# Kernel tuning notes

Measured on AMD Instinct MI355X. Metric: run time of the kernel, lower is better.

The kernel has to match this reference:

```python
import jax, jax.numpy as jnp
import numpy as np


def setup_inputs() -> dict:
    key = jax.random.key(0)
    ks = jax.random.split(key, 7)
    B, C, H, W = 8, 512, 32, 32
    N = 4
    Cn = C // N
    return {
        "first": jax.random.normal(ks[0], (B, C, H, W), dtype=jnp.float32),
        "second": jax.random.normal(ks[1], (B, C, H, W), dtype=jnp.float32),
        "w1": jax.random.normal(ks[2], (Cn, Cn), dtype=jnp.float32) * 0.05,
        "w2": jax.random.normal(ks[3], (Cn, Cn), dtype=jnp.float32) * 0.05,
        "w3": jax.random.normal(ks[4], (Cn, Cn), dtype=jnp.float32) * 0.05,
        "w4": jax.random.normal(ks[5], (Cn, Cn), dtype=jnp.float32) * 0.05,
        "w5": jax.random.normal(ks[6], (C, N), dtype=jnp.float32) * 0.05,
        "head_count": N,
    }


def reference(first, second, w1, w2, w3, w4, w5, head_count):
    B, C, H, W = first.shape
    N = head_count
    Cn = C // N
    L = H * W
    f = first.reshape(B * N, Cn, L)   # [BN, Cn, L]
    s = second.reshape(B * N, Cn, L)
    # 1x1 convs (no bias) == channel matmuls
    key_t = jnp.einsum('oc,bcl->blo', w1, f)    # [BN, L, Cn]
    query = jnp.einsum('oc,bcl->bol', w2, s)    # [BN, Cn, L]
    scores = jnp.einsum('blc,bcm->blm', key_t, query)  # [BN, L, L]
    attn = jax.nn.softmax(scores, axis=2)
    v1_t = jnp.einsum('oc,bcl->blo', w3, f)     # [BN, L, Cn]
    v2 = jnp.einsum('oc,bcl->bol', w4, s)       # [BN, Cn, L]
    value = jnp.einsum('blc,bcm->blm', v1_t, v2)  # [BN, L, L]
    res = jnp.sum(attn * value, axis=2)         # [BN, L]
    res = res.reshape(B, N, H, W)
    out = jax.nn.relu(jnp.einsum('on,bnhw->bohw', w5, res))  # [B, C, H, W]
    return out
```

## Files before the change

kernel.cpp:

```cpp
#include <hip/hip_runtime.h>
#include <hip/hip_bf16.h>
#include <stdint.h>

constexpr int BN = 32;
constexpr int Cn = 128;
constexpr int L  = 1024;
constexpr int CC = 512;
constexpr int BB = 8;

typedef __bf16 bf16x8 __attribute__((ext_vector_type(8)));
typedef float  f32x4  __attribute__((ext_vector_type(4)));
typedef unsigned short u16x8 __attribute__((ext_vector_type(8)));

__device__ inline unsigned short f2bf(float f) {
    unsigned int x = __float_as_uint(f);
    x += 0x7fffu + ((x >> 16) & 1u);
    return (unsigned short)(x >> 16);
}

__device__ inline void gl_lds16(const void* g, void* l) {
    typedef __attribute__((address_space(1))) const unsigned int GU;
    typedef __attribute__((address_space(3))) unsigned int LU;
    __builtin_amdgcn_global_load_lds((GU*)g, (LU*)l, 16, 0, 0);
}

__global__ __launch_bounds__(256)
void wsplit_kernel(const float* __restrict__ w1, const float* __restrict__ w2,
                   const float* __restrict__ w3, const float* __restrict__ w4,
                   unsigned short* __restrict__ whi, unsigned short* __restrict__ wlo)
{
    int idx = (blockIdx.x * 256 + threadIdx.x) * 4;
    int mat = idx >> 14;
    int off = idx & 16383;
    const float* w = (mat == 0) ? w1 : (mat == 1) ? w2 : (mat == 2) ? w3 : w4;
    float4 v = *(const float4*)&w[off];
    ushort4 hi, lo;
    hi.x = f2bf(v.x); lo.x = f2bf(v.x - __uint_as_float((unsigned)hi.x << 16));
    hi.y = f2bf(v.y); lo.y = f2bf(v.y - __uint_as_float((unsigned)hi.y << 16));
    hi.z = f2bf(v.z); lo.z = f2bf(v.z - __uint_as_float((unsigned)hi.z << 16));
    hi.w = f2bf(v.w); lo.w = f2bf(v.w - __uint_as_float((unsigned)hi.w << 16));
    *(ushort4*)&whi[idx] = hi;
    *(ushort4*)&wlo[idx] = lo;
}

__global__ __launch_bounds__(512, 2)
void proj_kernel(const float* __restrict__ first, const float* __restrict__ second,
                 const unsigned short* __restrict__ whi,
                 const unsigned short* __restrict__ wlo,
                 unsigned short* __restrict__ outP)
{
    __shared__ unsigned short xs[2][2][64 * 128];

    const int p   = blockIdx.x;
    const int lq  = p & 3;
    const int src = (p >> 2) & 1;
    const int bn  = p >> 3;

    const float* x = (src == 0 ? first : second) + (size_t)bn * Cn * L + lq * 256;

    const int tid  = threadIdx.x;
    const int lane = tid & 63;
    const int wv   = tid >> 6;
    const int mat  = wv & 1;
    const int oh   = (wv >> 1) & 1;
    const int lh   = wv >> 2;
    const int r16  = lane & 15;
    const int g    = lane >> 4;

    const int mi = mat * 2 + src;
    const unsigned short* WHm = whi + mi * 16384;
    const unsigned short* WLm = wlo + mi * 16384;
    unsigned short* Pout = outP + (size_t)(mi * BN + bn) * (L * Cn);

    bf16x8 ah[4][4], al[4][4];
    #pragma unroll
    for (int og = 0; og < 4; ++og)
        #pragma unroll
        for (int kk = 0; kk < 4; ++kk) {
            int o = oh * 64 + og * 16 + r16;
            int c = kk * 32 + g * 8;
            ah[og][kk] = *(const bf16x8*)&WHm[o * 128 + c];
            al[og][kk] = *(const bf16x8*)&WLm[o * 128 + c];
        }

    const int sl   = tid & 63;
    const int cblk = tid >> 6;

    float xf[16];
    auto PREF = [&](int s) {
        const float* xb = x + s * 64 + sl;
        #pragma unroll
        for (int j = 0; j < 16; ++j)
            xf[j] = xb[(size_t)(cblk * 16 + j) * L];
    };
    auto WRITE = [&](int buf) {
        #pragma unroll
        for (int half = 0; half < 2; ++half) {
            u16x8 hi, lo;
            #pragma unroll
            for (int j = 0; j < 8; ++j) {
                float v = xf[half * 8 + j];
                unsigned short h = f2bf(v);
                hi[j] = h;
                lo[j] = f2bf(v - __uint_as_float((unsigned)h << 16));
            }
            int chunk = cblk * 2 + half;
            int slot  = chunk ^ (sl & 15);
            int off   = sl * 128 + slot * 8;
            *(u16x8*)&xs[0][buf][off] = hi;
            *(u16x8*)&xs[1][buf][off] = lo;
        }
    };

    PREF(0);
    WRITE(0);
    __syncthreads();

    #pragma unroll
    for (int s = 0; s < 4; ++s) {
        const int buf = s & 1;
        if (s < 3) PREF(s + 1);

        f32x4 acc[4][2];
        #pragma unroll
        for (int a = 0; a < 4; ++a)
            #pragma unroll
            for (int b = 0; b < 2; ++b) acc[a][b] = (f32x4){0.f, 0.f, 0.f, 0.f};

        #pragma unroll
        for (int kk = 0; kk < 4; ++kk) {
            bf16x8 bh[2], bl[2];
            #pragma unroll
            for (int lg = 0; lg < 2; ++lg) {
                int l = lh * 32 + lg * 16 + r16;
                int slot = ((kk << 2) + g) ^ (l & 15);
                bh[lg] = *(const bf16x8*)&xs[0][buf][l * 128 + slot * 8];
                bl[lg] = *(const bf16x8*)&xs[1][buf][l * 128 + slot * 8];
            }
            #pragma unroll
            for (int og = 0; og < 4; ++og)
                #pragma unroll
                for (int lg = 0; lg < 2; ++lg) {
                    f32x4 a = acc[og][lg];
                    a = __builtin_amdgcn_mfma_f32_16x16x32_bf16(ah[og][kk], bh[lg], a, 0, 0, 0);
                    a = __builtin_amdgcn_mfma_f32_16x16x32_bf16(al[og][kk], bh[lg], a, 0, 0, 0);
                    a = __builtin_amdgcn_mfma_f32_16x16x32_bf16(ah[og][kk], bl[lg], a, 0, 0, 0);
                    acc[og][lg] = a;
                }
        }

        #pragma unroll
        for (int og = 0; og < 4; ++og)
            #pragma unroll
            for (int lg = 0; lg < 2; ++lg) {
                int o0 = oh * 64 + og * 16 + g * 4;
                int l  = lq * 256 + s * 64 + lh * 32 + lg * 16 + r16;
                f32x4 a = acc[og][lg];
                ushort4 st;
                st.x = f2bf(a.x); st.y = f2bf(a.y);
                st.z = f2bf(a.z); st.w = f2bf(a.w);
                int pos = (((o0 >> 3) ^ (l & 7)) << 3) | (o0 & 7);
                *(ushort4*)&Pout[(size_t)l * 128 + pos] = st;
            }

        if (s < 3) {
            WRITE(buf ^ 1);
            __syncthreads();
        }
    }
}

__global__ __launch_bounds__(256, 2)
void attn_kernel(const unsigned short* __restrict__ Pb,
                 float* __restrict__ Dp, float* __restrict__ Rp)
{
    __shared__ char smem[2][2][16384];

    const int p   = blockIdx.x;
    const int xcd = p & 7;
    const int jj  = p >> 3;
    const int bn  = xcd * 4 + (jj & 3);
    const int lt  = (jj >> 2) & 7;
    const int mh  = jj >> 5;

    const int tid  = threadIdx.x;
    const int lane = tid & 63;
    const int w    = tid >> 6;
    const int r16  = lane & 15;
    const int g    = lane >> 4;
    const int swz  = lane & 7;

    const size_t slab = (size_t)L * Cn;
    const unsigned short* Kt  = Pb + (size_t)(0 * BN + bn) * slab;
    const unsigned short* Qt  = Pb + (size_t)(1 * BN + bn) * slab;
    const unsigned short* V1t = Pb + (size_t)(2 * BN + bn) * slab;
    const unsigned short* V2t = Pb + (size_t)(3 * BN + bn) * slab;

    const int lbase = lt * 128;

    bf16x8 ka[2][4], va[2][4];
    #pragma unroll
    for (int i = 0; i < 2; ++i)
        #pragma unroll
        for (int kk = 0; kk < 4; ++kk) {
            int row = lbase + w * 32 + i * 16 + r16;
            int cp = ((kk << 2) + g) ^ swz;
            ka[i][kk] = *(const bf16x8*)(Kt  + (size_t)row * 128 + cp * 8);
            va[i][kk] = *(const bf16x8*)(V1t + (size_t)row * 128 + cp * 8);
        }

    const f32x4 z = {0.f, 0.f, 0.f, 0.f};
    f32x4 Dv[2] = {z, z};
    f32x4 Rv[2] = {z, z};

    auto STAGE = [&](int buf, int t) {
        const int m0 = mh * 512 + t * 64;
        const char* qs = (const char*)Qt  + (size_t)m0 * 256;
        const char* vs = (const char*)V2t + (size_t)m0 * 256;
        char* qd = &smem[buf][0][0];
        char* vd = &smem[buf][1][0];
        #pragma unroll
        for (int it = 0; it < 4; ++it) {
            gl_lds16(qs + tid * 16 + it * 4096, qd + tid * 16 + it * 4096);
            gl_lds16(vs + tid * 16 + it * 4096, vd + tid * 16 + it * 4096);
        }
    };

    auto COMPUTE = [&](int buf) {
        const char* qb = &smem[buf][0][0];
        const char* vb = &smem[buf][1][0];
        #pragma unroll
        for (int cg = 0; cg < 4; ++cg) {
            const int brow = cg * 16 + r16;
            const int rbase = brow * 256;
            bf16x8 qf[4], vf[4];
            #pragma unroll
            for (int kk = 0; kk < 4; ++kk) {
                int off = rbase + ((((kk << 2) + g) ^ swz) << 4);
                qf[kk] = *(const bf16x8*)(qb + off);
                vf[kk] = *(const bf16x8*)(vb + off);
            }
            f32x4 s0 = z, s1 = z, u0 = z, u1 = z;
            #pragma unroll
            for (int kk = 0; kk < 4; ++kk) {
                s0 = __builtin_amdgcn_mfma_f32_16x16x32_bf16(ka[0][kk], qf[kk], s0, 0, 0, 0);
                s1 = __builtin_amdgcn_mfma_f32_16x16x32_bf16(ka[1][kk], qf[kk], s1, 0, 0, 0);
                u0 = __builtin_amdgcn_mfma_f32_16x16x32_bf16(va[0][kk], vf[kk], u0, 0, 0, 0);
                u1 = __builtin_amdgcn_mfma_f32_16x16x32_bf16(va[1][kk], vf[kk], u1, 0, 0, 0);
            }
            f32x4 e0, e1;
            e0.x = __expf(s0.x - 8.f); e0.y = __expf(s0.y - 8.f);
            e0.z = __expf(s0.z - 8.f); e0.w = __expf(s0.w - 8.f);
            e1.x = __expf(s1.x - 8.f); e1.y = __expf(s1.y - 8.f);
            e1.z = __expf(s1.z - 8.f); e1.w = __expf(s1.w - 8.f);
            Dv[0] += e0;      Dv[1] += e1;
            Rv[0] += e0 * u0; Rv[1] += e1 * u1;
        }
    };

    STAGE(0, 0);
    __syncthreads();
    for (int t = 0; t < 8; ++t) {
        if (t < 7) STAGE((t + 1) & 1, t + 1);
        COMPUTE(t & 1);
        __syncthreads();
    }

    #pragma unroll
    for (int off = 8; off >= 1; off >>= 1) {
        #pragma unroll
        for (int i = 0; i < 2; ++i) {
            #pragma unroll
            for (int r = 0; r < 4; ++r) {
                Dv[i][r] += __shfl_xor(Dv[i][r], off);
                Rv[i][r] += __shfl_xor(Rv[i][r], off);
            }
        }
    }
    if (r16 == 0) {
        #pragma unroll
        for (int i = 0; i < 2; ++i)
            #pragma unroll
            for (int r = 0; r < 4; ++r) {
                int l = lbase + w * 32 + i * 16 + g * 4 + r;
                size_t idx = (size_t)mh * BN * L + (size_t)bn * L + l;
                Dp[idx] = Dv[i][r];
                Rp[idx] = Rv[i][r];
            }
    }
}

__global__ __launch_bounds__(256)
void combine_kernel(const float* __restrict__ Dp, const float* __restrict__ Rp,
                    float* __restrict__ res)
{
    int i = blockIdx.x * 256 + threadIdx.x;
    float d = Dp[i] + Dp[BN * L + i];
    float r = Rp[i] + Rp[BN * L + i];
    res[i] = r / d;
}

__global__ __launch_bounds__(256)
void out_kernel(const float* __restrict__ res, const float* __restrict__ w5,
                float* __restrict__ out)
{
    const int blk = blockIdx.x;
    const int o = blk & 511;
    const int b = blk >> 9;
    const float4 wv = *(const float4*)&w5[o * 4];

    const float* r0 = res + (size_t)(b * 4 + 0) * L;
    const float* r1 = res + (size_t)(b * 4 + 1) * L;
    const float* r2 = res + (size_t)(b * 4 + 2) * L;
    const float* r3 = res + (size_t)(b * 4 + 3) * L;

    const int hw = threadIdx.x * 4;
    float4 a0 = *(const float4*)&r0[hw];
    float4 a1 = *(const float4*)&r1[hw];
    float4 a2 = *(const float4*)&r2[hw];
    float4 a3 = *(const float4*)&r3[hw];

    float4 ov;
    ov.x = fmaxf(0.f, wv.x * a0.x + wv.y * a1.x + wv.z * a2.x + wv.w * a3.x);
    ov.y = fmaxf(0.f, wv.x * a0.y + wv.y * a1.y + wv.z * a2.y + wv.w * a3.y);
    ov.z = fmaxf(0.f, wv.x * a0.z + wv.y * a1.z + wv.z * a2.z + wv.w * a3.z);
    ov.w = fmaxf(0.f, wv.x * a0.w + wv.y * a1.w + wv.z * a2.w + wv.w * a3.w);

    *(float4*)&out[(size_t)blk * 1024 + hw] = ov;
}

extern "C" void kernel_launch(void* const* d_in, const int* in_sizes, int n_in,
                              void* d_out, int out_size, void* d_ws, size_t ws_size,
                              hipStream_t stream)
{
    const float* first  = (const float*)d_in[0];
    const float* second = (const float*)d_in[1];
    const float* w1 = (const float*)d_in[2];
    const float* w2 = (const float*)d_in[3];
    const float* w3 = (const float*)d_in[4];
    const float* w4 = (const float*)d_in[5];
    const float* w5 = (const float*)d_in[6];
    float* out = (float*)d_out;

    const size_t projBytes = (size_t)4 * BN * L * Cn * sizeof(unsigned short);
    unsigned short* P = (unsigned short*)d_ws;
    float* Dp  = (float*)((char*)d_ws + projBytes);
    float* Rp  = Dp + 2 * BN * L;
    float* res = Rp + 2 * BN * L;
    unsigned short* whi = (unsigned short*)(res + BN * L);
    unsigned short* wlo = whi + 4 * 16384;

    wsplit_kernel<<<dim3(64), dim3(256), 0, stream>>>(w1, w2, w3, w4, whi, wlo);
    proj_kernel<<<dim3(256), dim3(512), 0, stream>>>(first, second, whi, wlo, P);
    attn_kernel<<<dim3(512), dim3(256), 0, stream>>>(P, Dp, Rp);
    combine_kernel<<<dim3(BN * L / 256), dim3(256), 0, stream>>>(Dp, Rp, res);
    out_kernel<<<dim3(BB * CC), dim3(256), 0, stream>>>(res, w5, out);
}
```

Measured before the change: 63.35 us.

## Pre-split inputs to bf16 hi/lo in a separate pass and stage via global_load_lds

Moves the fp32-to-bf16 hi/lo split of the input activations out of the projection kernel into a combined split kernel that also splits the weights. The split writes swizzled, L-major layouts to workspace. The projection kernel then stages tiles straight into LDS with global_load_lds, uses smaller L tiles and output-channel halves per wave, and doubles the grid with higher occupancy. This removes strided fp32 loads and conversion work from the MFMA kernel, but adds a full extra write and read of the split activations through global memory.

```diff
diff --git a/kernel.cpp b/kernel.cpp
--- a/kernel.cpp
+++ b/kernel.cpp
@@ -25,45 +25,87 @@
 }
 
 __global__ __launch_bounds__(256)
-void wsplit_kernel(const float* __restrict__ w1, const float* __restrict__ w2,
+void xsplit_kernel(const float* __restrict__ first, const float* __restrict__ second,
+                   const float* __restrict__ w1, const float* __restrict__ w2,
                    const float* __restrict__ w3, const float* __restrict__ w4,
+                   unsigned short* __restrict__ xhi, unsigned short* __restrict__ xlo,
                    unsigned short* __restrict__ whi, unsigned short* __restrict__ wlo)
 {
-    int idx = (blockIdx.x * 256 + threadIdx.x) * 4;
-    int mat = idx >> 14;
-    int off = idx & 16383;
-    const float* w = (mat == 0) ? w1 : (mat == 1) ? w2 : (mat == 2) ? w3 : w4;
-    float4 v = *(const float4*)&w[off];
-    ushort4 hi, lo;
-    hi.x = f2bf(v.x); lo.x = f2bf(v.x - __uint_as_float((unsigned)hi.x << 16));
-    hi.y = f2bf(v.y); lo.y = f2bf(v.y - __uint_as_float((unsigned)hi.y << 16));
-    hi.z = f2bf(v.z); lo.z = f2bf(v.z - __uint_as_float((unsigned)hi.z << 16));
-    hi.w = f2bf(v.w); lo.w = f2bf(v.w - __uint_as_float((unsigned)hi.w << 16));
-    *(ushort4*)&whi[idx] = hi;
-    *(ushort4*)&wlo[idx] = lo;
-}
-
-__global__ __launch_bounds__(512, 2)
-void proj_kernel(const float* __restrict__ first, const float* __restrict__ second,
+    const int blk = blockIdx.x;
+    const int t   = threadIdx.x;
+
+    if (blk >= 1024) {
+        int idx = ((blk - 1024) * 256 + t) * 4;
+        int mat = idx >> 14;
+        int off = idx & 16383;
+        const float* w = (mat == 0) ? w1 : (mat == 1) ? w2 : (mat == 2) ? w3 : w4;
+        float4 v = *(const float4*)&w[off];
+        ushort4 hi, lo;
+        hi.x = f2bf(v.x); lo.x = f2bf(v.x - __uint_as_float((unsigned)hi.x << 16));
+        hi.y = f2bf(v.y); lo.y = f2bf(v.y - __uint_as_float((unsigned)hi.y << 16));
+        hi.z = f2bf(v.z); lo.z = f2bf(v.z - __uint_as_float((unsigned)hi.z << 16));
+        hi.w = f2bf(v.w); lo.w = f2bf(v.w - __uint_as_float((unsigned)hi.w << 16));
+        *(ushort4*)&whi[idx] = hi;
+        *(ushort4*)&wlo[idx] = lo;
+        return;
+    }
+
+    const int slab   = blk >> 4;
+    const int lchunk = blk & 15;
+    const int src    = slab >> 5;
+    const int bn     = slab & 31;
+    const float* xs = (src ? second : first) + (size_t)bn * Cn * L;
+
+    const int l     = t & 63;
+    const int q     = t >> 6;
+    const int lg    = lchunk * 64 + l;
+    const size_t rowbase = (size_t)slab * (L * Cn) + (size_t)lg * Cn;
+
+    #pragma unroll
+    for (int i = 0; i < 4; ++i) {
+        const int coct = q * 4 + i;
+        float v[8];
+        #pragma unroll
+        for (int j = 0; j < 8; ++j)
+            v[j] = xs[(size_t)(coct * 8 + j) * L + lg];
+        u16x8 hi, lo;
+        #pragma unroll
+        for (int j = 0; j < 8; ++j) {
+            unsigned short h = f2bf(v[j]);
+            hi[j] = h;
+            lo[j] = f2bf(v[j] - __uint_as_float((unsigned)h << 16));
+        }
+        const int pos = (coct ^ (lg & 15)) * 8;
+        *(u16x8*)&xhi[rowbase + pos] = hi;
+        *(u16x8*)&xlo[rowbase + pos] = lo;
+    }
+}
+
+__global__ __launch_bounds__(512, 4)
+void proj_kernel(const unsigned short* __restrict__ xhi,
+                 const unsigned short* __restrict__ xlo,
                  const unsigned short* __restrict__ whi,
                  const unsigned short* __restrict__ wlo,
                  unsigned short* __restrict__ outP)
 {
-    __shared__ unsigned short xs[2][2][64 * 128];
+    __shared__ unsigned short xh[2][32 * 128];
+    __shared__ unsigned short xl[2][32 * 128];
 
     const int p   = blockIdx.x;
-    const int lq  = p & 3;
-    const int src = (p >> 2) & 1;
-    const int bn  = p >> 3;
-
-    const float* x = (src == 0 ? first : second) + (size_t)bn * Cn * L + lq * 256;
+    const int lt  = p & 7;
+    const int src = (p >> 3) & 1;
+    const int bn  = p >> 4;
+
+    const int slab = src * 32 + bn;
+    const unsigned short* XH = xhi + (size_t)slab * (L * Cn);
+    const unsigned short* XL = xlo + (size_t)slab * (L * Cn);
 
     const int tid  = threadIdx.x;
     const int lane = tid & 63;
-    const int wv   = tid >> 6;
-    const int mat  = wv & 1;
-    const int oh   = (wv >> 1) & 1;
-    const int lh   = wv >> 2;
+    const int wid  = tid >> 6;
+    const int mat  = wid & 1;
+    const int oh   = (wid >> 1) & 1;
+    const int ogh  = wid >> 2;
     const int r16  = lane & 15;
     const int g    = lane >> 4;
 
@@ -72,58 +114,36 @@
     const unsigned short* WLm = wlo + mi * 16384;
     unsigned short* Pout = outP + (size_t)(mi * BN + bn) * (L * Cn);
 
-    bf16x8 ah[4][4], al[4][4];
-    #pragma unroll
-    for (int og = 0; og < 4; ++og)
+    const int obase = oh * 64 + ogh * 32;
+
+    bf16x8 ah[2][4], al[2][4];
+    #pragma unroll
+    for (int og = 0; og < 2; ++og)
         #pragma unroll
         for (int kk = 0; kk < 4; ++kk) {
-            int o = oh * 64 + og * 16 + r16;
+            int o = obase + og * 16 + r16;
             int c = kk * 32 + g * 8;
             ah[og][kk] = *(const bf16x8*)&WHm[o * 128 + c];
             al[og][kk] = *(const bf16x8*)&WLm[o * 128 + c];
         }
 
-    const int sl   = tid & 63;
-    const int cblk = tid >> 6;
-
-    float xf[16];
-    auto PREF = [&](int s) {
-        const float* xb = x + s * 64 + sl;
-        #pragma unroll
-        for (int j = 0; j < 16; ++j)
-            xf[j] = xb[(size_t)(cblk * 16 + j) * L];
+    auto STAGE = [&](int buf, int s) {
+        const size_t src_off = ((size_t)(lt * 128 + s * 32)) * Cn + tid * 8;
+        gl_lds16(XH + src_off, &xh[buf][tid * 8]);
+        gl_lds16(XL + src_off, &xl[buf][tid * 8]);
     };
-    auto WRITE = [&](int buf) {
-        #pragma unroll
-        for (int half = 0; half < 2; ++half) {
-            u16x8 hi, lo;
-            #pragma unroll
-            for (int j = 0; j < 8; ++j) {
-                float v = xf[half * 8 + j];
-                unsigned short h = f2bf(v);
-                hi[j] = h;
-                lo[j] = f2bf(v - __uint_as_float((unsigned)h << 16));
-            }
-            int chunk = cblk * 2 + half;
-            int slot  = chunk ^ (sl & 15);
-            int off   = sl * 128 + slot * 8;
-            *(u16x8*)&xs[0][buf][off] = hi;
-            *(u16x8*)&xs[1][buf][off] = lo;
-        }
-    };
-
-    PREF(0);
-    WRITE(0);
+
+    STAGE(0, 0);
     __syncthreads();
 
     #pragma unroll
     for (int s = 0; s < 4; ++s) {
         const int buf = s & 1;
-        if (s < 3) PREF(s + 1);
-
-        f32x4 acc[4][2];
-        #pragma unroll
-        for (int a = 0; a < 4; ++a)
+        if (s < 3) STAGE(buf ^ 1, s + 1);
+
+        f32x4 acc[2][2];
+        #pragma unroll
+        for (int a = 0; a < 2; ++a)
             #pragma unroll
             for (int b = 0; b < 2; ++b) acc[a][b] = (f32x4){0.f, 0.f, 0.f, 0.f};
 
@@ -132,13 +152,13 @@
             bf16x8 bh[2], bl[2];
             #pragma unroll
             for (int lg = 0; lg < 2; ++lg) {
-                int l = lh * 32 + lg * 16 + r16;
-                int slot = ((kk << 2) + g) ^ (l & 15);
-                bh[lg] = *(const bf16x8*)&xs[0][buf][l * 128 + slot * 8];
-                bl[lg] = *(const bf16x8*)&xs[1][buf][l * 128 + slot * 8];
-            }
-            #pragma unroll
-            for (int og = 0; og < 4; ++og)
+                int row  = lg * 16 + r16;
+                int slot = ((kk << 2) + g) ^ r16;
+                bh[lg] = *(const bf16x8*)&xh[buf][row * 128 + slot * 8];
+                bl[lg] = *(const bf16x8*)&xl[buf][row * 128 + slot * 8];
+            }
+            #pragma unroll
+            for (int og = 0; og < 2; ++og)
                 #pragma unroll
                 for (int lg = 0; lg < 2; ++lg) {
                     f32x4 a = acc[og][lg];
@@ -150,11 +170,11 @@
         }
 
         #pragma unroll
-        for (int og = 0; og < 4; ++og)
+        for (int og = 0; og < 2; ++og)
             #pragma unroll
             for (int lg = 0; lg < 2; ++lg) {
-                int o0 = oh * 64 + og * 16 + g * 4;
-                int l  = lq * 256 + s * 64 + lh * 32 + lg * 16 + r16;
+                int o0 = obase + og * 16 + g * 4;
+                int l  = lt * 128 + s * 32 + lg * 16 + r16;
                 f32x4 a = acc[og][lg];
                 ushort4 st;
                 st.x = f2bf(a.x); st.y = f2bf(a.y);
@@ -163,10 +183,7 @@
                 *(ushort4*)&Pout[(size_t)l * 128 + pos] = st;
             }
 
-        if (s < 3) {
-            WRITE(buf ^ 1);
-            __syncthreads();
-        }
+        __syncthreads();
     }
 }
 
@@ -342,16 +359,20 @@
     const float* w5 = (const float*)d_in[6];
     float* out = (float*)d_out;
 
-    const size_t projBytes = (size_t)4 * BN * L * Cn * sizeof(unsigned short);
-    unsigned short* P = (unsigned short*)d_ws;
+    const size_t slabElems = (size_t)L * Cn;
+    const size_t projBytes = (size_t)4 * BN * slabElems * 2;
+    unsigned short* P   = (unsigned short*)d_ws;
     float* Dp  = (float*)((char*)d_ws + projBytes);
     float* Rp  = Dp + 2 * BN * L;
     float* res = Rp + 2 * BN * L;
     unsigned short* whi = (unsigned short*)(res + BN * L);
     unsigned short* wlo = whi + 4 * 16384;
-
-    wsplit_kernel<<<dim3(64), dim3(256), 0, stream>>>(w1, w2, w3, w4, whi, wlo);
-    proj_kernel<<<dim3(256), dim3(512), 0, stream>>>(first, second, whi, wlo, P);
+    unsigned short* xhi = wlo + 4 * 16384;
+    unsigned short* xlo = xhi + 64 * slabElems;
+
+    xsplit_kernel<<<dim3(1088), dim3(256), 0, stream>>>(
+        first, second, w1, w2, w3, w4, xhi, xlo, whi, wlo);
+    proj_kernel<<<dim3(512), dim3(512), 0, stream>>>(xhi, xlo, whi, wlo, P);
     attn_kernel<<<dim3(512), dim3(256), 0, stream>>>(P, Dp, Rp);
     combine_kernel<<<dim3(BN * L / 256), dim3(256), 0, stream>>>(Dp, Rp, res);
     out_kernel<<<dim3(BB * CC), dim3(256), 0, stream>>>(res, w5, out);
```

Result: slower. 74.54 us (+17.7%).
